# Kernel optimization log

Hardware: AMD Instinct MI355X
Metric: run time of the kernel (lower is better)

## Reference

```python
import jax, jax.numpy as jnp
import numpy as np

B, S, D = 64, 512, 768  # batch, max wordpieces (BERT max pos), hidden dim


def setup_inputs() -> dict:
    key = jax.random.key(0)
    k_emb, k_seg = jax.random.split(key)
    # last_hidden_state from the (frozen) BERT backbone
    embeddings = jax.random.normal(k_emb, (B, S, D), dtype=jnp.float32)
    # word-group id per wordpiece token, non-decreasing within each row
    # (token i belongs to word segment_ids[b, i]; '##' continuations share
    #  the id of their head wordpiece, mirroring aggregate_tokens)
    segment_ids = jnp.sort(
        jax.random.randint(k_seg, (B, S), 0, S, dtype=jnp.int32), axis=-1
    )
    return {"embeddings": embeddings, "segment_ids": segment_ids}


def reference(embeddings, segment_ids):
    # Vectorized equivalent of BertEncoder.aggregate_tokens + head slicing:
    # sum wordpiece embeddings within each word group, zero-pad to S words.
    n, s, d = embeddings.shape
    agg = jax.vmap(
        lambda e, seg: jax.ops.segment_sum(e, seg, num_segments=s)
    )(embeddings, segment_ids)  # [B, S, D], trailing unused slots are zeros
    report_feat = agg[:, 0]      # [B, D]   ([CLS] word embedding)
    word_feat = agg[:, 1:]       # [B, S-1, D]
    return report_feat, word_feat
```

## Files before the change

kernel.cpp:

```cpp
#include <hip/hip_runtime.h>


typedef float v4f __attribute__((ext_vector_type(4)));

constexpr int B  = 64;
constexpr int S  = 512;
constexpr int D  = 768;
constexpr int D4 = D / 4;
constexpr int G  = 4;
constexpr int BLOCK = 256;

__global__ __launch_bounds__(BLOCK) void segsum_r5_kernel(
    const v4f* __restrict__ emb,
    const int* __restrict__ seg,
    v4f*       __restrict__ out) {
  const int wave = (blockIdx.x * BLOCK + threadIdx.x) >> 6;
  const int lane = threadIdx.x & 63;
  const int b    = wave >> 7;
  const int g0   = (wave & 127) << 2;

  const int4* row = (const int4*)(seg + b * S);
  const int4 a0 = row[lane];
  const int4 a1 = row[lane + 64];

  int bnd[G + 1];
#pragma unroll
  for (int k = 0; k <= G; ++k) {
    const int t = g0 + k;
    int c = 0;
    c += __popcll(__ballot(a0.x < t));
    c += __popcll(__ballot(a0.y < t));
    c += __popcll(__ballot(a0.z < t));
    c += __popcll(__ballot(a0.w < t));
    c += __popcll(__ballot(a1.x < t));
    c += __popcll(__ballot(a1.y < t));
    c += __popcll(__ballot(a1.z < t));
    c += __popcll(__ballot(a1.w < t));
    bnd[k] = c;
  }

  const v4f* base = emb + (size_t)b * S * D4 + lane;

  v4f q[G][3];
#pragma unroll
  for (int k = 0; k < G; ++k) {
    if (bnd[k] < bnd[k + 1]) {
      const v4f* p = base + (size_t)bnd[k] * D4;
      q[k][0] = p[0];
      q[k][1] = p[64];
      q[k][2] = p[128];
    }
  }

  const v4f zero = {0.f, 0.f, 0.f, 0.f};
#pragma unroll
  for (int k = 0; k < G; ++k) {
    if (bnd[k] >= bnd[k + 1]) {
      q[k][0] = zero; q[k][1] = zero; q[k][2] = zero;
    } else {
      for (int s = bnd[k] + 1; s < bnd[k + 1]; ++s) {
        const v4f* p = base + (size_t)s * D4;
        v4f e0 = p[0], e1 = p[64], e2 = p[128];
        q[k][0] += e0; q[k][1] += e1; q[k][2] += e2;
      }
    }
    const int g = g0 + k;
    v4f* dst = (g == 0)
        ? out + (size_t)b * D4
        : out + (size_t)B * D4 + ((size_t)b * (S - 1) + (g - 1)) * D4;
    __builtin_nontemporal_store(q[k][0], dst + lane);
    __builtin_nontemporal_store(q[k][1], dst + lane + 64);
    __builtin_nontemporal_store(q[k][2], dst + lane + 128);
  }
}

extern "C" void kernel_launch(void* const* d_in, const int* in_sizes, int n_in,
                              void* d_out, int out_size, void* d_ws, size_t ws_size,
                              hipStream_t stream) {
  const v4f* emb = (const v4f*)d_in[0];
  const int* seg = (const int*)d_in[1];
  v4f*       out = (v4f*)d_out;

  const int waves  = B * S / G;
  const int blocks = waves / (BLOCK / 64);
  segsum_r5_kernel<<<blocks, BLOCK, 0, stream>>>(emb, seg, out);
}
```

Before: 182.2 us.

## Split segment work across more waves and stage segment ids in LDS

Each block now covers one batch row's slice. Its four waves each handle two non-adjacent groups (g and g+256) instead of one wave handling four consecutive groups, which doubles the number of waves launched. The segment-id row is loaded once per block into shared memory and then read by all waves, instead of each wave reading it from global memory. The goal is more memory-level parallelism and better load balance in a latency-bound gather-sum. The cost is a block barrier and fewer first-row loads in flight per wave.

Result: no change. 179.3 us (-1.5%).

```diff
diff --git a/kernel.cpp b/kernel.cpp
--- a/kernel.cpp
+++ b/kernel.cpp
@@ -5,28 +5,36 @@
 
 constexpr int B  = 64;
 constexpr int S  = 512;
-constexpr int D  = 768;
-constexpr int D4 = D / 4;
-constexpr int G  = 4;
+constexpr int D4 = 192;
 constexpr int BLOCK = 256;
 
-__global__ __launch_bounds__(BLOCK) void segsum_r5_kernel(
+__global__ __launch_bounds__(BLOCK) void segsum_r6_kernel(
     const v4f* __restrict__ emb,
     const int* __restrict__ seg,
     v4f*       __restrict__ out) {
-  const int wave = (blockIdx.x * BLOCK + threadIdx.x) >> 6;
+  __shared__ int4 sm[S / 4];
+
+  const int blk  = blockIdx.x;
+  const int b    = blk >> 6;
+  const int j    = blk & 63;
+  const int wv   = threadIdx.x >> 6;
   const int lane = threadIdx.x & 63;
-  const int b    = wave >> 7;
-  const int g0   = (wave & 127) << 2;
 
-  const int4* row = (const int4*)(seg + b * S);
-  const int4 a0 = row[lane];
-  const int4 a1 = row[lane + 64];
+  if (threadIdx.x < S / 4)
+    sm[threadIdx.x] = ((const int4*)(seg + b * S))[threadIdx.x];
+  __syncthreads();
 
-  int bnd[G + 1];
+  const int4 a0 = sm[lane];
+  const int4 a1 = sm[lane + 64];
+
+  const int g0 = 4 * j + wv;
+  const int g1 = g0 + 256;
+
+  const int tg[4] = {g0, g0 + 1, g1, g1 + 1};
+  int lb[4];
 #pragma unroll
-  for (int k = 0; k <= G; ++k) {
-    const int t = g0 + k;
+  for (int i = 0; i < 4; ++i) {
+    const int t = tg[i];
     int c = 0;
     c += __popcll(__ballot(a0.x < t));
     c += __popcll(__ballot(a0.y < t));
@@ -36,41 +44,46 @@
     c += __popcll(__ballot(a1.y < t));
     c += __popcll(__ballot(a1.z < t));
     c += __popcll(__ballot(a1.w < t));
-    bnd[k] = c;
+    lb[i] = c;
   }
 
   const v4f* base = emb + (size_t)b * S * D4 + lane;
+  const v4f zero = {0.f, 0.f, 0.f, 0.f};
+  const bool ne0 = lb[0] < lb[1];
+  const bool ne1 = lb[2] < lb[3];
 
-  v4f q[G][3];
-#pragma unroll
-  for (int k = 0; k < G; ++k) {
-    if (bnd[k] < bnd[k + 1]) {
-      const v4f* p = base + (size_t)bnd[k] * D4;
-      q[k][0] = p[0];
-      q[k][1] = p[64];
-      q[k][2] = p[128];
+  v4f q0a, q0b, q0c, q1a, q1b, q1c;
+  if (ne0) { const v4f* p = base + (size_t)lb[0] * D4; q0a = p[0]; q0b = p[64]; q0c = p[128]; }
+  if (ne1) { const v4f* p = base + (size_t)lb[2] * D4; q1a = p[0]; q1b = p[64]; q1c = p[128]; }
+
+  if (!ne0) { q0a = zero; q0b = zero; q0c = zero; }
+  else {
+    for (int s = lb[0] + 1; s < lb[1]; ++s) {
+      const v4f* p = base + (size_t)s * D4;
+      q0a += p[0]; q0b += p[64]; q0c += p[128];
     }
   }
+  {
+    v4f* dst = (g0 == 0)
+        ? out + (size_t)b * D4
+        : out + (size_t)B * D4 + ((size_t)b * (S - 1) + (g0 - 1)) * D4;
+    __builtin_nontemporal_store(q0a, dst + lane);
+    __builtin_nontemporal_store(q0b, dst + lane + 64);
+    __builtin_nontemporal_store(q0c, dst + lane + 128);
+  }
 
-  const v4f zero = {0.f, 0.f, 0.f, 0.f};
-#pragma unroll
-  for (int k = 0; k < G; ++k) {
-    if (bnd[k] >= bnd[k + 1]) {
-      q[k][0] = zero; q[k][1] = zero; q[k][2] = zero;
-    } else {
-      for (int s = bnd[k] + 1; s < bnd[k + 1]; ++s) {
-        const v4f* p = base + (size_t)s * D4;
-        v4f e0 = p[0], e1 = p[64], e2 = p[128];
-        q[k][0] += e0; q[k][1] += e1; q[k][2] += e2;
-      }
+  if (!ne1) { q1a = zero; q1b = zero; q1c = zero; }
+  else {
+    for (int s = lb[2] + 1; s < lb[3]; ++s) {
+      const v4f* p = base + (size_t)s * D4;
+      q1a += p[0]; q1b += p[64]; q1c += p[128];
     }
-    const int g = g0 + k;
-    v4f* dst = (g == 0)
-        ? out + (size_t)b * D4
-        : out + (size_t)B * D4 + ((size_t)b * (S - 1) + (g - 1)) * D4;
-    __builtin_nontemporal_store(q[k][0], dst + lane);
-    __builtin_nontemporal_store(q[k][1], dst + lane + 64);
-    __builtin_nontemporal_store(q[k][2], dst + lane + 128);
+  }
+  {
+    v4f* dst = out + (size_t)B * D4 + ((size_t)b * (S - 1) + (g1 - 1)) * D4;
+    __builtin_nontemporal_store(q1a, dst + lane);
+    __builtin_nontemporal_store(q1b, dst + lane + 64);
+    __builtin_nontemporal_store(q1c, dst + lane + 128);
   }
 }
 
@@ -81,7 +94,6 @@
   const int* seg = (const int*)d_in[1];
   v4f*       out = (v4f*)d_out;
 
-  const int waves  = B * S / G;
-  const int blocks = waves / (BLOCK / 64);
-  segsum_r5_kernel<<<blocks, BLOCK, 0, stream>>>(emb, seg, out);
+  const int blocks = B * 64;
+  segsum_r6_kernel<<<blocks, BLOCK, 0, stream>>>(emb, seg, out);
 }
```
